# Kernel optimization log

Hardware: AMD Instinct MI355X
Metric: run time of the kernel (lower is better)

## Reference

```python
import jax, jax.numpy as jnp
import numpy as np

B, S, D = 2, 2048, 1024
H = 16
HD = D // H  # head_dim = 64


def setup_inputs() -> dict:
    key = jax.random.key(0)
    ks = jax.random.split(key, 6)
    scale = 0.02
    x = jax.random.normal(ks[0], (B, S, D), dtype=jnp.float32)
    Wq = jax.random.normal(ks[1], (D, D), dtype=jnp.float32) * scale
    Wk = jax.random.normal(ks[2], (D, D), dtype=jnp.float32) * scale
    Wv = jax.random.normal(ks[3], (D, D), dtype=jnp.float32) * scale
    Wo = jax.random.normal(ks[4], (D, D), dtype=jnp.float32) * scale
    bo = jax.random.normal(ks[5], (D,), dtype=jnp.float32) * scale
    return {"x": x, "Wq": Wq, "Wk": Wk, "Wv": Wv, "Wo": Wo, "bo": bo}


def reference(x, Wq, Wk, Wv, Wo, bo):
    b, s, d = x.shape
    # QKV projections (no bias, qkv_bias=False)
    Q = (x @ Wq).reshape(b, s, H, HD)
    K = (x @ Wk).reshape(b, s, H, HD)
    V = (x @ Wv).reshape(b, s, H, HD)
    # [b, h, q, k] attention scores
    scores = jnp.einsum('bqhd,bkhd->bhqk', Q, K)
    # causal mask: positions k > q masked to -inf (applied before scaling, as in source;
    # -inf / sqrt(hd) is still -inf so this matches)
    causal = jnp.triu(jnp.ones((s, s), dtype=bool), k=1)
    scores = jnp.where(causal, -jnp.inf, scores)
    att = jax.nn.softmax(scores / jnp.sqrt(jnp.float32(HD)), axis=-1)
    # dropout p=0.0 -> identity
    ctx = jnp.einsum('bhqk,bkhd->bqhd', att, V).reshape(b, s, d)
    return ctx @ Wo + bo
```

## Files before the change

### kernel.cpp

```cpp
#include <hip/hip_runtime.h>

typedef __bf16 bf16;
typedef __attribute__((ext_vector_type(8))) __bf16 bf16x8;
typedef __attribute__((ext_vector_type(4))) __bf16 bf16x4;
typedef __attribute__((ext_vector_type(4))) float floatx4;

#define MFMA16(a, b, c) __builtin_amdgcn_mfma_f32_16x16x32_bf16((a), (b), (c), 0, 0, 0)

static constexpr int BB = 2, SS = 2048, DD = 1024, HH = 16;
static constexpr int MM = BB * SS;
static constexpr int N_QKV = 3 * DD;

__device__ __forceinline__ float exp2c(float x) {
#if __has_builtin(__builtin_amdgcn_exp2f)
    return __builtin_amdgcn_exp2f(x);
#else
    return exp2f(x);
#endif
}

__device__ __forceinline__ void async16(const void* g, void* l) {
    __builtin_amdgcn_global_load_lds(
        (const __attribute__((address_space(1))) unsigned int*)g,
        (__attribute__((address_space(3))) unsigned int*)l, 16, 0, 0);
}

__global__ __launch_bounds__(256) void prep_kernel(const float* __restrict__ x,
                                                   bf16* __restrict__ xb,
                                                   const float* __restrict__ w0,
                                                   const float* __restrict__ w1,
                                                   const float* __restrict__ w2,
                                                   const float* __restrict__ w3,
                                                   bf16* __restrict__ outT) {
    const int blk = blockIdx.x, tid = threadIdx.x;
    if (blk < 4096) {
        int i = blk * 1024 + tid * 4;
        float4 v = *(const float4*)(x + i);
        bf16x4 o;
        o[0] = (bf16)v.x; o[1] = (bf16)v.y; o[2] = (bf16)v.z; o[3] = (bf16)v.w;
        *(bf16x4*)(xb + i) = o;
    } else {
        __shared__ float tile[32][33];
        const int wblk = blk - 4096;
        const int z = wblk >> 10, rem = wblk & 1023;
        const int by = rem >> 5, bx = rem & 31;
        const float* src = (z == 0) ? w0 : (z == 1) ? w1 : (z == 2) ? w2 : w3;
        bf16* dst = outT + (size_t)z * DD * DD;
        const int y0 = by * 32, x0 = bx * 32;
        {
            const int tx = tid & 7, ty = tid >> 3;
            float4 v = *(const float4*)(src + (size_t)(y0 + ty) * DD + x0 + tx * 4);
            tile[ty][tx * 4 + 0] = v.x;
            tile[ty][tx * 4 + 1] = v.y;
            tile[ty][tx * 4 + 2] = v.z;
            tile[ty][tx * 4 + 3] = v.w;
        }
        __syncthreads();
        {
            const int tx = tid & 7, c = tid >> 3;
            bf16x4 o;
            o[0] = (bf16)tile[tx * 4 + 0][c];
            o[1] = (bf16)tile[tx * 4 + 1][c];
            o[2] = (bf16)tile[tx * 4 + 2][c];
            o[3] = (bf16)tile[tx * 4 + 3][c];
            *(bf16x4*)(dst + (size_t)(x0 + c) * DD + y0 + tx * 4) = o;
        }
    }
}

template <int BM, int BN, bool OUT_BF16, bool FUSE_VT>
__global__ __launch_bounds__(256) void gemm_kernel(const bf16* __restrict__ A,
                                                   const bf16* __restrict__ Bt,
                                                   void* __restrict__ C,
                                                   bf16* __restrict__ Vt_g,
                                                   const float* __restrict__ bias,
                                                   int K, int ldc) {
    constexpr int MT = BM / 32, NT = BN / 32;
    __shared__ bf16 As[BM * 64];
    __shared__ bf16 Bs[BN * 64];
    const int tid = threadIdx.x, wave = tid >> 6, lane = tid & 63;
    const int quad = lane >> 4, l16 = lane & 15;
    const int wm = wave >> 1, wn = wave & 1;
    const int m0 = blockIdx.y * BM, n0 = blockIdx.x * BN;
    const int l8r = lane >> 3, l8c = lane & 7;
    const int gch = ((l8c ^ l8r) * 8);

    floatx4 acc[MT][NT] = {};

    for (int k0 = 0; k0 < K; k0 += 64) {
        __syncthreads();
#pragma unroll
        for (int c = 0; c < BM / 32; ++c) {
            int r = wave * (BM / 4) + c * 8;
            async16(A + (size_t)(m0 + r + l8r) * K + k0 + gch, &As[r * 64]);
        }
#pragma unroll
        for (int c = 0; c < BN / 32; ++c) {
            int r = wave * (BN / 4) + c * 8;
            async16(Bt + (size_t)(n0 + r + l8r) * K + k0 + gch, &Bs[r * 64]);
        }
        __syncthreads();
#pragma unroll
        for (int cc = 0; cc < 2; ++cc) {
            bf16x8 af[MT], bv[NT];
#pragma unroll
            for (int i = 0; i < MT; ++i) {
                int row = wm * (BM / 2) + i * 16 + l16;
                af[i] = *(const bf16x8*)&As[row * 64 + ((cc * 4 + quad) ^ (row & 7)) * 8];
            }
#pragma unroll
            for (int j = 0; j < NT; ++j) {
                int row = wn * (BN / 2) + j * 16 + l16;
                bv[j] = *(const bf16x8*)&Bs[row * 64 + ((cc * 4 + quad) ^ (row & 7)) * 8];
            }
#pragma unroll
            for (int i = 0; i < MT; ++i)
#pragma unroll
                for (int j = 0; j < NT; ++j)
                    acc[i][j] = MFMA16(af[i], bv[j], acc[i][j]);
        }
    }

    if (FUSE_VT && n0 >= 2048) {
#pragma unroll
        for (int i = 0; i < MT; ++i)
#pragma unroll
            for (int j = 0; j < NT; ++j) {
                int grow = m0 + wm * (BM / 2) + i * 16 + quad * 4;
                int gcol = n0 + wn * (BN / 2) + j * 16 + l16;
                int bb = grow >> 11, s = grow & (SS - 1);
                int vcol = gcol - 2048;
                int hh = vcol >> 6, hd = vcol & 63;
                bf16x4 pk;
#pragma unroll
                for (int r = 0; r < 4; ++r) pk[r] = (bf16)acc[i][j][r];
                *(bf16x4*)&Vt_g[(((size_t)(bb * 16 + hh)) * 64 + hd) * SS + s] = pk;
            }
        return;
    }

#pragma unroll
    for (int i = 0; i < MT; ++i)
#pragma unroll
        for (int j = 0; j < NT; ++j)
#pragma unroll
            for (int r = 0; r < 4; ++r) {
                int row = m0 + wm * (BM / 2) + i * 16 + quad * 4 + r;
                int col = n0 + wn * (BN / 2) + j * 16 + l16;
                if (OUT_BF16)
                    ((bf16*)C)[(size_t)row * ldc + col] = (bf16)acc[i][j][r];
                else
                    ((float*)C)[(size_t)row * ldc + col] = acc[i][j][r] + bias[col];
            }
}

__global__ __launch_bounds__(256, 4) void attn_kernel(const bf16* __restrict__ QKV,
                                                      const bf16* __restrict__ Vt_g,
                                                      bf16* __restrict__ ctx) {
    __shared__ __align__(16) bf16 smem[20480];
    bf16* Ks = smem;
    bf16* Vt = smem + 8192;
    bf16* Ps = smem + 16384;
    bf16* Qs = Ps;

    const int tid = threadIdx.x, wave = tid >> 6, lane = tid & 63;
    const int quad = lane >> 4, l16 = lane & 15;
    const int gb = blockIdx.x;
    const int xcd = gb & 7, rr = gb >> 3;
    const int hi = rr >> 5, lo = rr & 31;
    const int t = (hi == 0) ? lo : (hi == 1) ? (31 - lo)
                : (hi == 2) ? (lo ^ 16) : (31 - (lo ^ 16));
    const int bh = xcd * 4 + hi;
    const int b = bh >> 4, h = bh & 15;
    const int q0 = t * 64;
    const size_t base = (size_t)(b * SS) * N_QKV;
    const bf16* Vg = Vt_g + (size_t)bh * 64 * SS;
    constexpr float C2 = 0.18033688011112042f;
    const int l8r = lane >> 3, l8c = lane & 7;
    const int gch = (l8c ^ l8r) * 8;
    const int swz = l16 & 7;
    const int nkt = t + 1;

    {
#pragma unroll
        for (int c = 0; c < 2; ++c) {
            int r0 = wave * 16 + c * 8;
            async16(QKV + base + (size_t)(q0 + r0 + l8r) * N_QKV + h * 64 + gch,
                    Qs + r0 * 64);
            async16(QKV + base + (size_t)(r0 + l8r) * N_QKV + DD + h * 64 + gch,
                    Ks + r0 * 64);
            async16(Vg + (size_t)(r0 + l8r) * SS + gch, Vt + r0 * 64);
        }
    }
    __syncthreads();

    bf16x8 qf[2];
#pragma unroll
    for (int cc = 0; cc < 2; ++cc) {
        int row = wave * 16 + l16;
        qf[cc] = *(const bf16x8*)&Qs[row * 64 + ((cc * 4 + quad) ^ swz) * 8];
    }

    bf16x8 onesf = {};
    if (l16 == 0) {
#pragma unroll
        for (int e = 0; e < 8; ++e) onesf[e] = (bf16)1.0f;
    }

    floatx4 accv[4] = {};
    floatx4 acc5 = {};
    const int qg = q0 + wave * 16 + l16;

    for (int kt = 0; kt < nkt; ++kt) {
        const int buf = kt & 1;
        if (kt + 1 < nkt) {
            const int k0n = (kt + 1) * 64;
            const int dst = (buf ^ 1) * 4096;
#pragma unroll
            for (int c = 0; c < 2; ++c) {
                int r0 = wave * 16 + c * 8;
                async16(QKV + base + (size_t)(k0n + r0 + l8r) * N_QKV + DD + h * 64 + gch,
                        Ks + dst + r0 * 64);
                async16(Vg + (size_t)(r0 + l8r) * SS + k0n + gch, Vt + dst + r0 * 64);
            }
        }
        const int k0 = kt * 64;

        floatx4 st[4];
#pragma unroll
        for (int j = 0; j < 4; ++j) st[j] = (floatx4){};
        __builtin_amdgcn_s_setprio(1);
#pragma unroll
        for (int cc = 0; cc < 2; ++cc)
#pragma unroll
            for (int j = 0; j < 4; ++j) {
                bf16x8 kf = *(const bf16x8*)&Ks[buf * 4096 + (j * 16 + l16) * 64
                                                + ((cc * 4 + quad) ^ swz) * 8];
                st[j] = MFMA16(kf, qf[cc], st[j]);
            }
        __builtin_amdgcn_s_setprio(0);

        if (kt == nkt - 1) {
#pragma unroll
            for (int j = 0; j < 4; ++j) {
                int kb = k0 + j * 16 + quad * 4;
#pragma unroll
                for (int r = 0; r < 4; ++r)
                    if (kb + r > qg) st[j][r] = -__builtin_inff();
            }
        }

#pragma unroll
        for (int j = 0; j < 4; ++j) {
            bf16x4 pk4;
#pragma unroll
            for (int r = 0; r < 4; ++r)
                pk4[r] = (bf16)exp2c(st[j][r] * C2);
            *(bf16x4*)&Ps[wave * 1024 + l16 * 64
                          + ((2 * j + (quad >> 1)) ^ swz) * 8 + (quad & 1) * 4] = pk4;
        }

        bf16x8 pf[2];
#pragma unroll
        for (int cc = 0; cc < 2; ++cc)
            pf[cc] = *(const bf16x8*)&Ps[wave * 1024 + l16 * 64
                                         + ((cc * 4 + quad) ^ swz) * 8];
        __builtin_amdgcn_s_setprio(1);
#pragma unroll
        for (int cc = 0; cc < 2; ++cc)
#pragma unroll
            for (int j = 0; j < 4; ++j) {
                bf16x8 vt = *(const bf16x8*)&Vt[buf * 4096 + (j * 16 + l16) * 64
                                                + ((cc * 4 + quad) ^ swz) * 8];
                accv[j] = MFMA16(pf[cc], vt, accv[j]);
            }
        acc5 = MFMA16(pf[0], onesf, acc5);
        acc5 = MFMA16(pf[1], onesf, acc5);
        __builtin_amdgcn_s_setprio(0);

        __syncthreads();
    }

    float inv[4];
#pragma unroll
    for (int r = 0; r < 4; ++r)
        inv[r] = 1.0f / __shfl(acc5[r], lane & 48, 64);
#pragma unroll
    for (int j = 0; j < 4; ++j)
#pragma unroll
        for (int r = 0; r < 4; ++r) {
            int row = b * SS + q0 + wave * 16 + quad * 4 + r;
            int col = h * 64 + j * 16 + l16;
            ctx[(size_t)row * DD + col] = (bf16)(accv[j][r] * inv[r]);
        }
}

extern "C" void kernel_launch(void* const* d_in, const int* in_sizes, int n_in,
                              void* d_out, int out_size, void* d_ws, size_t ws_size,
                              hipStream_t stream) {
    const float* x  = (const float*)d_in[0];
    const float* Wq = (const float*)d_in[1];
    const float* Wk = (const float*)d_in[2];
    const float* Wv = (const float*)d_in[3];
    const float* Wo = (const float*)d_in[4];
    const float* bo = (const float*)d_in[5];
    float* out = (float*)d_out;

    char* ws = (char*)d_ws;
    bf16* xb   = (bf16*)ws;
    bf16* WT   = (bf16*)(ws + (size_t)(8  << 20));
    bf16* QKV  = (bf16*)(ws + (size_t)(16 << 20));
    bf16* ctxb = (bf16*)(ws + (size_t)(40 << 20));
    bf16* Vt_g = (bf16*)(ws + (size_t)(48 << 20));

    prep_kernel<<<dim3(8192), dim3(256), 0, stream>>>(x, xb, Wq, Wk, Wv, Wo, WT);
    gemm_kernel<128, 128, true, true><<<dim3(N_QKV / 128, MM / 128), dim3(256), 0, stream>>>(
        xb, WT, QKV, Vt_g, nullptr, DD, N_QKV);
    attn_kernel<<<dim3(1024), dim3(256), 0, stream>>>(QKV, Vt_g, ctxb);
    gemm_kernel<128, 64, false, false><<<dim3(DD / 64, MM / 128), dim3(256), 0, stream>>>(
        ctxb, WT + (size_t)3 * DD * DD, out, nullptr, bo, DD, DD);
}
```

Before: 167.2 us.

## Replace QKV projection GEMM with 256x256-tile, 512-thread double-buffered kernel

Adds a new GEMM kernel for the QKV projection that uses 256x256 output tiles, 8 waves and double-buffered LDS. The global-to-LDS async loads for the next k-step are interleaved with MFMA quarters, synchronised by explicit vmcnt waits and barriers. The larger tile is meant to raise arithmetic intensity and cut global traffic, and the interleaving is meant to hide load latency. In exchange the grid shrinks to 12x16=192 blocks, which may underfill the 256 CUs, and register and LDS pressure rise (64KB+ LDS).

```diff
diff --git a/kernel.cpp b/kernel.cpp
--- a/kernel.cpp
+++ b/kernel.cpp
@@ -154,6 +154,156 @@
             }
 }
 
+template <bool FUSE_VT>
+__global__ __launch_bounds__(512, 2) void gemm256_kernel(const bf16* __restrict__ A,
+                                                         const bf16* __restrict__ Bt,
+                                                         bf16* __restrict__ C,
+                                                         bf16* __restrict__ Vt_g,
+                                                         int K, int ldc) {
+    __shared__ __align__(16) bf16 As[2 * 256 * 64];
+    __shared__ __align__(16) bf16 Bs[2 * 256 * 64];
+    const int tid = threadIdx.x, wave = tid >> 6, lane = tid & 63;
+    const int quad = lane >> 4, l16 = lane & 15;
+    const int wm = wave >> 2, wn = wave & 3;
+    const int m0 = blockIdx.y * 256, n0 = blockIdx.x * 256;
+    const int l8r = lane >> 3, l8c = lane & 7;
+    const int gch = (l8c ^ l8r) * 8;
+    const int nk = K >> 6;
+
+    floatx4 acc[2][4][2][2] = {};
+    bf16x8 af[4][2], bn0[2][2], bn1[2][2];
+
+#define VMW4 asm volatile("s_waitcnt vmcnt(4)" ::: "memory")
+#define VMW2 asm volatile("s_waitcnt vmcnt(2)" ::: "memory")
+#define VMW0 asm volatile("s_waitcnt vmcnt(0)" ::: "memory")
+#define BARX __builtin_amdgcn_s_barrier()
+
+#define STAGE_A(H, KN, BUF)                                                       \
+    {                                                                             \
+        _Pragma("unroll") for (int c = 0; c < 2; ++c) {                           \
+            int r0 = (H) * 128 + c * 64 + wave * 8;                               \
+            async16(A + (size_t)(m0 + r0 + l8r) * K + (KN) + gch,                 \
+                    &As[(BUF) * 16384 + r0 * 64]);                                \
+        }                                                                         \
+    }
+#define STAGE_B(H, KN, BUF)                                                       \
+    {                                                                             \
+        _Pragma("unroll") for (int c = 0; c < 2; ++c) {                           \
+            int r0 = (H) * 128 + c * 64 + wave * 8;                               \
+            async16(Bt + (size_t)(n0 + r0 + l8r) * K + (KN) + gch,                \
+                    &Bs[(BUF) * 16384 + r0 * 64]);                                \
+        }                                                                         \
+    }
+#define READ_A(MH, BUF)                                                           \
+    {                                                                             \
+        _Pragma("unroll") for (int m = 0; m < 4; ++m) {                           \
+            int row = (MH) * 128 + wm * 64 + m * 16 + l16;                        \
+            _Pragma("unroll") for (int kk = 0; kk < 2; ++kk)                      \
+                af[m][kk] = *(const bf16x8*)&As[(BUF) * 16384 + row * 64 +        \
+                                               (((kk * 4 + quad) ^ (row & 7)) * 8)]; \
+        }                                                                         \
+    }
+#define READ_B(DST, NH, BUF)                                                      \
+    {                                                                             \
+        _Pragma("unroll") for (int n = 0; n < 2; ++n) {                           \
+            int row = (NH) * 128 + wn * 32 + n * 16 + l16;                        \
+            _Pragma("unroll") for (int kk = 0; kk < 2; ++kk)                      \
+                DST[n][kk] = *(const bf16x8*)&Bs[(BUF) * 16384 + row * 64 +       \
+                                                (((kk * 4 + quad) ^ (row & 7)) * 8)]; \
+        }                                                                         \
+    }
+#define MMAC(MH, NH, BF)                                                          \
+    {                                                                             \
+        __builtin_amdgcn_s_setprio(1);                                            \
+        _Pragma("unroll") for (int m = 0; m < 4; ++m)                             \
+            _Pragma("unroll") for (int n = 0; n < 2; ++n)                         \
+                _Pragma("unroll") for (int kk = 0; kk < 2; ++kk)                  \
+                    acc[MH][m][NH][n] =                                           \
+                        MFMA16(af[m][kk], BF[n][kk], acc[MH][m][NH][n]);          \
+        __builtin_amdgcn_s_setprio(0);                                            \
+    }
+
+    STAGE_A(0, 0, 0);
+    STAGE_B(0, 0, 0);
+    STAGE_B(1, 0, 0);
+    STAGE_A(1, 0, 0);
+
+    for (int kt = 0; kt < nk; ++kt) {
+        const int buf = kt & 1;
+        const int knext = (kt + 1) << 6;
+        const bool last = (kt == nk - 1);
+
+        VMW4;
+        BARX;
+        READ_A(0, buf);
+        READ_B(bn0, 0, buf);
+        if (!last) STAGE_A(0, knext, buf ^ 1);
+        MMAC(0, 0, bn0);
+
+        if (!last) { VMW4; } else { VMW2; }
+        BARX;
+        READ_B(bn1, 1, buf);
+        if (!last) STAGE_B(0, knext, buf ^ 1);
+        MMAC(0, 1, bn1);
+
+        if (!last) { VMW4; } else { VMW0; }
+        BARX;
+        READ_A(1, buf);
+        if (!last) STAGE_B(1, knext, buf ^ 1);
+        MMAC(1, 0, bn0);
+
+        if (!last) STAGE_A(1, knext, buf ^ 1);
+        MMAC(1, 1, bn1);
+    }
+
+#undef VMW4
+#undef VMW2
+#undef VMW0
+#undef BARX
+#undef STAGE_A
+#undef STAGE_B
+#undef READ_A
+#undef READ_B
+#undef MMAC
+
+    if (FUSE_VT && n0 >= 2048) {
+#pragma unroll
+        for (int mh = 0; mh < 2; ++mh)
+#pragma unroll
+            for (int m = 0; m < 4; ++m)
+#pragma unroll
+                for (int nh = 0; nh < 2; ++nh)
+#pragma unroll
+                    for (int n = 0; n < 2; ++n) {
+                        int grow = m0 + mh * 128 + wm * 64 + m * 16 + quad * 4;
+                        int gcol = n0 + nh * 128 + wn * 32 + n * 16 + l16;
+                        int bb = grow >> 11, s = grow & (SS - 1);
+                        int vcol = gcol - 2048;
+                        int hh = vcol >> 6, hd = vcol & 63;
+                        bf16x4 pk;
+#pragma unroll
+                        for (int r = 0; r < 4; ++r) pk[r] = (bf16)acc[mh][m][nh][n][r];
+                        *(bf16x4*)&Vt_g[(((size_t)(bb * 16 + hh)) * 64 + hd) * SS + s] = pk;
+                    }
+        return;
+    }
+
+#pragma unroll
+    for (int mh = 0; mh < 2; ++mh)
+#pragma unroll
+        for (int m = 0; m < 4; ++m)
+#pragma unroll
+            for (int nh = 0; nh < 2; ++nh)
+#pragma unroll
+                for (int n = 0; n < 2; ++n)
+#pragma unroll
+                    for (int r = 0; r < 4; ++r) {
+                        int row = m0 + mh * 128 + wm * 64 + m * 16 + quad * 4 + r;
+                        int col = n0 + nh * 128 + wn * 32 + n * 16 + l16;
+                        C[(size_t)row * ldc + col] = (bf16)acc[mh][m][nh][n][r];
+                    }
+}
+
 __global__ __launch_bounds__(256, 4) void attn_kernel(const bf16* __restrict__ QKV,
                                                       const bf16* __restrict__ Vt_g,
                                                       bf16* __restrict__ ctx) {
@@ -314,8 +464,8 @@
     bf16* Vt_g = (bf16*)(ws + (size_t)(48 << 20));
 
     prep_kernel<<<dim3(8192), dim3(256), 0, stream>>>(x, xb, Wq, Wk, Wv, Wo, WT);
-    gemm_kernel<128, 128, true, true><<<dim3(N_QKV / 128, MM / 128), dim3(256), 0, stream>>>(
-        xb, WT, QKV, Vt_g, nullptr, DD, N_QKV);
+    gemm256_kernel<true><<<dim3(N_QKV / 256, MM / 256), dim3(512), 0, stream>>>(
+        xb, WT, QKV, Vt_g, DD, N_QKV);
     attn_kernel<<<dim3(1024), dim3(256), 0, stream>>>(QKV, Vt_g, ctxb);
     gemm_kernel<128, 64, false, false><<<dim3(DD / 64, MM / 128), dim3(256), 0, stream>>>(
         ctxb, WT + (size_t)3 * DD * DD, out, nullptr, bo, DD, DD);
```

After: 170.5 us. About the same (+1.9%).

## Replace QKV GEMM with 256x192 double-buffered, 512-thread pipelined kernel

Applied to the files above, without the earlier changes.

The QKV projection moves to a new kernel with 256x192 tiles, 8 waves, and double-buffered LDS filled by async global-to-LDS loads. Loads for the next k-step are issued while MFMAs for the current step run, with explicit vmcnt waits and raised wave priority around the MFMA blocks. The aim is to hide global-load latency and get more reuse per LDS tile. In exchange the grid shrinks to 16x16=256 blocks, which roughly matches the CU count and may leave a partial wave, and LDS use grows to about 112KB per block.

```diff
diff --git a/kernel.cpp b/kernel.cpp
--- a/kernel.cpp
+++ b/kernel.cpp
@@ -68,11 +68,10 @@
     }
 }
 
-template <int BM, int BN, bool OUT_BF16, bool FUSE_VT>
+template <int BM, int BN, bool OUT_BF16>
 __global__ __launch_bounds__(256) void gemm_kernel(const bf16* __restrict__ A,
                                                    const bf16* __restrict__ Bt,
                                                    void* __restrict__ C,
-                                                   bf16* __restrict__ Vt_g,
                                                    const float* __restrict__ bias,
                                                    int K, int ldc) {
     constexpr int MT = BM / 32, NT = BN / 32;
@@ -121,24 +120,6 @@
         }
     }
 
-    if (FUSE_VT && n0 >= 2048) {
-#pragma unroll
-        for (int i = 0; i < MT; ++i)
-#pragma unroll
-            for (int j = 0; j < NT; ++j) {
-                int grow = m0 + wm * (BM / 2) + i * 16 + quad * 4;
-                int gcol = n0 + wn * (BN / 2) + j * 16 + l16;
-                int bb = grow >> 11, s = grow & (SS - 1);
-                int vcol = gcol - 2048;
-                int hh = vcol >> 6, hd = vcol & 63;
-                bf16x4 pk;
-#pragma unroll
-                for (int r = 0; r < 4; ++r) pk[r] = (bf16)acc[i][j][r];
-                *(bf16x4*)&Vt_g[(((size_t)(bb * 16 + hh)) * 64 + hd) * SS + s] = pk;
-            }
-        return;
-    }
-
 #pragma unroll
     for (int i = 0; i < MT; ++i)
 #pragma unroll
@@ -151,6 +132,126 @@
                     ((bf16*)C)[(size_t)row * ldc + col] = (bf16)acc[i][j][r];
                 else
                     ((float*)C)[(size_t)row * ldc + col] = acc[i][j][r] + bias[col];
+            }
+}
+
+__global__ __launch_bounds__(512, 2) void gemm192_kernel(const bf16* __restrict__ A,
+                                                         const bf16* __restrict__ Bt,
+                                                         bf16* __restrict__ C,
+                                                         bf16* __restrict__ Vt_g,
+                                                         int K, int ldc) {
+    __shared__ __align__(16) bf16 As[2 * 256 * 64];
+    __shared__ __align__(16) bf16 Bs[2 * 192 * 64];
+    const int tid = threadIdx.x, wave = tid >> 6, lane = tid & 63;
+    const int quad = lane >> 4, l16 = lane & 15;
+    const int wm = wave >> 2, wn = wave & 3;
+    const int m0 = blockIdx.y * 256, n0 = blockIdx.x * 192;
+    const int l8r = lane >> 3, l8c = lane & 7;
+    const int gch = (l8c ^ l8r) * 8;
+    const int nk = K >> 6;
+
+    floatx4 acc[2][4][3] = {};
+    bf16x8 af[4][2], bn[3][2];
+
+#define VMW(N) asm volatile("s_waitcnt vmcnt(" #N ")" ::: "memory")
+#define BARX __builtin_amdgcn_s_barrier()
+
+#define STAGE_A(H, KN, BUF)                                                       \
+    {                                                                             \
+        _Pragma("unroll") for (int c = 0; c < 2; ++c) {                           \
+            int r0 = (H) * 128 + c * 64 + wave * 8;                               \
+            async16(A + (size_t)(m0 + r0 + l8r) * K + (KN) + gch,                 \
+                    &As[(BUF) * 16384 + r0 * 64]);                                \
+        }                                                                         \
+    }
+#define STAGE_B(KN, BUF)                                                          \
+    {                                                                             \
+        _Pragma("unroll") for (int c = 0; c < 3; ++c) {                           \
+            int r0 = wave * 24 + c * 8;                                           \
+            async16(Bt + (size_t)(n0 + r0 + l8r) * K + (KN) + gch,                \
+                    &Bs[(BUF) * 12288 + r0 * 64]);                                \
+        }                                                                         \
+    }
+#define READ_A(MH, BUF)                                                           \
+    {                                                                             \
+        _Pragma("unroll") for (int m = 0; m < 4; ++m) {                           \
+            int row = (MH) * 128 + wm * 64 + m * 16 + l16;                        \
+            _Pragma("unroll") for (int kk = 0; kk < 2; ++kk)                      \
+                af[m][kk] = *(const bf16x8*)&As[(BUF) * 16384 + row * 64 +        \
+                                               (((kk * 4 + quad) ^ (row & 7)) * 8)]; \
+        }                                                                         \
+    }
+#define READ_B(BUF)                                                               \
+    {                                                                             \
+        _Pragma("unroll") for (int n = 0; n < 3; ++n) {                           \
+            int row = wn * 48 + n * 16 + l16;                                     \
+            _Pragma("unroll") for (int kk = 0; kk < 2; ++kk)                      \
+                bn[n][kk] = *(const bf16x8*)&Bs[(BUF) * 12288 + row * 64 +        \
+                                               (((kk * 4 + quad) ^ (row & 7)) * 8)]; \
+        }                                                                         \
+    }
+#define MMAC(MH)                                                                  \
+    {                                                                             \
+        __builtin_amdgcn_s_setprio(1);                                            \
+        _Pragma("unroll") for (int m = 0; m < 4; ++m)                             \
+            _Pragma("unroll") for (int n = 0; n < 3; ++n)                         \
+                _Pragma("unroll") for (int kk = 0; kk < 2; ++kk)                  \
+                    acc[MH][m][n] = MFMA16(af[m][kk], bn[n][kk], acc[MH][m][n]);  \
+        __builtin_amdgcn_s_setprio(0);                                            \
+    }
+
+    STAGE_A(0, 0, 0);
+    STAGE_B(0, 0);
+    STAGE_A(1, 0, 0);
+
+    for (int kt = 0; kt < nk; ++kt) {
+        const int buf = kt & 1;
+        const int knext = (kt + 1) << 6;
+        const bool last = (kt == nk - 1);
+
+        VMW(2);
+        BARX;
+        READ_A(0, buf);
+        READ_B(buf);
+        if (!last) { STAGE_A(0, knext, buf ^ 1); STAGE_B(knext, buf ^ 1); }
+        MMAC(0);
+
+        if (!last) { VMW(5); } else { VMW(0); }
+        BARX;
+        READ_A(1, buf);
+        if (!last) STAGE_A(1, knext, buf ^ 1);
+        MMAC(1);
+    }
+
+#undef VMW
+#undef BARX
+#undef STAGE_A
+#undef STAGE_B
+#undef READ_A
+#undef READ_B
+#undef MMAC
+
+#pragma unroll
+    for (int mh = 0; mh < 2; ++mh)
+#pragma unroll
+        for (int m = 0; m < 4; ++m)
+#pragma unroll
+            for (int n = 0; n < 3; ++n) {
+                int grow = m0 + mh * 128 + wm * 64 + m * 16 + quad * 4;
+                int gcol0 = n0 + wn * 48 + n * 16;
+                if (gcol0 >= 2048) {
+                    int bb = grow >> 11, s = grow & (SS - 1);
+                    int vcol = gcol0 + l16 - 2048;
+                    int hh = vcol >> 6, hd = vcol & 63;
+                    bf16x4 pk;
+#pragma unroll
+                    for (int r = 0; r < 4; ++r) pk[r] = (bf16)acc[mh][m][n][r];
+                    *(bf16x4*)&Vt_g[(((size_t)(bb * 16 + hh)) * 64 + hd) * SS + s] = pk;
+                } else {
+#pragma unroll
+                    for (int r = 0; r < 4; ++r)
+                        C[(size_t)(grow + r) * ldc + gcol0 + l16] = (bf16)acc[mh][m][n][r];
+                }
             }
 }
 
@@ -314,9 +415,9 @@
     bf16* Vt_g = (bf16*)(ws + (size_t)(48 << 20));
 
     prep_kernel<<<dim3(8192), dim3(256), 0, stream>>>(x, xb, Wq, Wk, Wv, Wo, WT);
-    gemm_kernel<128, 128, true, true><<<dim3(N_QKV / 128, MM / 128), dim3(256), 0, stream>>>(
-        xb, WT, QKV, Vt_g, nullptr, DD, N_QKV);
+    gemm192_kernel<<<dim3(N_QKV / 192, MM / 256), dim3(512), 0, stream>>>(
+        xb, WT, QKV, Vt_g, DD, N_QKV);
     attn_kernel<<<dim3(1024), dim3(256), 0, stream>>>(QKV, Vt_g, ctxb);
-    gemm_kernel<128, 64, false, false><<<dim3(DD / 64, MM / 128), dim3(256), 0, stream>>>(
-        ctxb, WT + (size_t)3 * DD * DD, out, nullptr, bo, DD, DD);
-}
+    gemm_kernel<128, 64, false><<<dim3(DD / 64, MM / 128), dim3(256), 0, stream>>>(
+        ctxb, WT + (size_t)3 * DD * DD, out, bo, DD, DD);
+}
```

Result: faster. 162.8 us (-2.7%).
